# Kernel optimization log

Measured on AMD Instinct MI355X. Metric: run time of the kernel, lower is better.

## Reference

```python
import jax, jax.numpy as jnp
import numpy as np

B, N1, N2, D, H = 16, 1024, 1024, 1024, 16
DH = D // H  # head dim = 64
NEG = jnp.float32(-1e30)  # mask fill value (avoids -inf NaNs, bf16-safe)


def setup_inputs() -> dict:
    key = jax.random.key(0)
    ks = jax.random.split(key, 8)
    s = 0.02
    q = jax.random.normal(ks[0], (B, N1, D), dtype=jnp.float32)
    x = jax.random.normal(ks[1], (B, N2, D), dtype=jnp.float32)
    Wq = jax.random.normal(ks[2], (D, D), dtype=jnp.float32) * s
    Wk = jax.random.normal(ks[3], (D, D), dtype=jnp.float32) * s
    Wv = jax.random.normal(ks[4], (D, D), dtype=jnp.float32) * s
    Wo = jax.random.normal(ks[5], (D, D), dtype=jnp.float32) * s
    bq = jnp.zeros((D,), jnp.float32)
    bk = jnp.zeros((D,), jnp.float32)
    bv = jnp.zeros((D,), jnp.float32)
    bo = jnp.zeros((D,), jnp.float32)
    adj_mat = jax.random.randint(ks[6], (N1, N2), 0, 2).astype(jnp.bool_)
    return {"q": q, "x": x, "Wq": Wq, "bq": bq, "Wk": Wk, "bk": bk,
            "Wv": Wv, "bv": bv, "Wo": Wo, "bo": bo, "adj_mat": adj_mat}


def reference(q, x, Wq, bq, Wk, bk, Wv, bv, Wo, bo, adj_mat):
    b = q.shape[0]
    # QKV projections (torch Linear: y = x @ W.T + b), split into heads
    qh = (q @ Wq.T + bq).reshape(b, N1, H, DH).transpose(0, 2, 1, 3)  # [B,H,N1,DH]
    kh = (x @ Wk.T + bk).reshape(b, N2, H, DH).transpose(0, 2, 1, 3)  # [B,H,N2,DH]
    vh = (x @ Wv.T + bv).reshape(b, N2, H, DH).transpose(0, 2, 1, 3)  # [B,H,N2,DH]
    # masked SDPA with fixed adjacency mask (broadcast over batch & heads)
    scale = jnp.asarray(DH, qh.dtype) ** -0.5
    scores = jnp.einsum("bhqd,bhkd->bhqk", qh, kh) * scale           # [B,H,N1,N2]
    scores = jnp.where(adj_mat, scores, NEG)
    attn = jax.nn.softmax(scores, axis=-1)
    o = jnp.einsum("bhqk,bhkd->bhqd", attn, vh)                      # [B,H,N1,DH]
    o = o.transpose(0, 2, 1, 3).reshape(b, N1, D)
    return o @ Wo.T + bo
```

## Files before the change

### kernel.cpp

```cpp
#include <hip/hip_runtime.h>


typedef float f32x4 __attribute__((ext_vector_type(4)));
typedef __bf16 bf16x8 __attribute__((ext_vector_type(8)));

#define QSCALE 0.18033688f

__device__ __forceinline__ unsigned short f2bf(float f) {
    unsigned u = __builtin_bit_cast(unsigned, f);
    unsigned r = u + 0x7fffu + ((u >> 16) & 1u);
    return (unsigned short)(r >> 16);
}
__device__ __forceinline__ unsigned pk2(float a, float b) {
    return (unsigned)f2bf(a) | ((unsigned)f2bf(b) << 16);
}

__global__ __launch_bounds__(256) void cvt_bf16(const float* __restrict__ src,
                                                unsigned short* __restrict__ dst,
                                                int n8) {
    const int idx = blockIdx.x * 256 + threadIdx.x;
    if (idx >= n8) return;
    float4 a = ((const float4*)src)[idx * 2];
    float4 b = ((const float4*)src)[idx * 2 + 1];
    uint4 u;
    u.x = pk2(a.x, a.y); u.y = pk2(a.z, a.w);
    u.z = pk2(b.x, b.y); u.w = pk2(b.z, b.w);
    ((uint4*)dst)[idx] = u;
}

__global__ __launch_bounds__(256) void cvt_w4(const float* __restrict__ W0,
                                              const float* __restrict__ W1,
                                              const float* __restrict__ W2,
                                              const float* __restrict__ W3,
                                              unsigned short* __restrict__ o0,
                                              unsigned short* __restrict__ o1,
                                              unsigned short* __restrict__ o2,
                                              unsigned short* __restrict__ o3) {
    const float* s = (blockIdx.y == 0) ? W0 : (blockIdx.y == 1) ? W1
                   : (blockIdx.y == 2) ? W2 : W3;
    unsigned short* d = (blockIdx.y == 0) ? o0 : (blockIdx.y == 1) ? o1
                      : (blockIdx.y == 2) ? o2 : o3;
    const int idx = blockIdx.x * 256 + threadIdx.x;
    float4 a = ((const float4*)s)[idx * 2];
    float4 b = ((const float4*)s)[idx * 2 + 1];
    uint4 u;
    u.x = pk2(a.x, a.y); u.y = pk2(a.z, a.w);
    u.z = pk2(b.x, b.y); u.w = pk2(b.z, b.w);
    ((uint4*)d)[idx] = u;
}

template <int OUTM>
__global__ __launch_bounds__(256) void gemm_lds(const unsigned short* __restrict__ A,
                                                const unsigned short* __restrict__ W,
                                                const float* __restrict__ bias,
                                                void* __restrict__ Cp,
                                                float scale) {
    constexpr int N = 1024, K = 1024;
    __shared__ unsigned short As[128 * 64];
    __shared__ unsigned short Bs[128 * 64];

    const int t    = threadIdx.x;
    const int wave = t >> 6;
    const int lane = t & 63;
    const int bid  = blockIdx.x;
    const int xcd  = bid & 7;
    const int jj   = bid >> 3;
    const int n0   = (jj & 7) * 128;
    const int m0   = (xcd * 16 + (jj >> 3)) * 128;
    const int wr   = (wave >> 1) * 64;
    const int wc   = (wave & 1) * 64;
    const int lm   = lane & 15;
    const int quad = lane >> 4;

    int aoff[4], boff[4];
#pragma unroll
    for (int i = 0; i < 4; i++) {
        const int slot = wave * 256 + i * 64 + lane;
        const int r = slot >> 3;
        const int csrc = (slot & 7) ^ (r & 7);
        aoff[i] = (m0 + r) * K + csrc * 8;
        boff[i] = (n0 + r) * K + csrc * 8;
    }

    f32x4 acc[4][4] = {};

    for (int k0 = 0; k0 < K; k0 += 64) {
#pragma unroll
        for (int i = 0; i < 4; i++) {
            __builtin_amdgcn_global_load_lds(
                (const __attribute__((address_space(1))) unsigned int*)(A + aoff[i] + k0),
                (__attribute__((address_space(3))) unsigned int*)((char*)As + wave * 4096 + i * 1024),
                16, 0, 0);
            __builtin_amdgcn_global_load_lds(
                (const __attribute__((address_space(1))) unsigned int*)(W + boff[i] + k0),
                (__attribute__((address_space(3))) unsigned int*)((char*)Bs + wave * 4096 + i * 1024),
                16, 0, 0);
        }
        __syncthreads();

        bf16x8 af[2][4], bfr[2][4];
#pragma unroll
        for (int ks = 0; ks < 2; ks++)
#pragma unroll
            for (int i = 0; i < 4; i++) {
                const int pos = ((ks * 4 + quad) ^ (lm & 7)) * 16;
                af[ks][i]  = *(const bf16x8*)((const char*)As + (wr + i * 16 + lm) * 128 + pos);
                bfr[ks][i] = *(const bf16x8*)((const char*)Bs + (wc + i * 16 + lm) * 128 + pos);
            }
#pragma unroll
        for (int ks = 0; ks < 2; ks++)
#pragma unroll
            for (int i = 0; i < 4; i++)
#pragma unroll
                for (int j = 0; j < 4; j++)
                    acc[i][j] = __builtin_amdgcn_mfma_f32_16x16x32_bf16(af[ks][i], bfr[ks][j],
                                                                        acc[i][j], 0, 0, 0);
        __syncthreads();
    }

#pragma unroll
    for (int i = 0; i < 4; i++) {
        const int row = m0 + wr + i * 16 + quad * 4;
#pragma unroll
        for (int j = 0; j < 4; j++) {
            const int col = n0 + wc + j * 16 + lm;
            const float bb = bias[col];
            if constexpr (OUTM == 2) {
                const int bi = row >> 10, n2 = row & 1023;
                const int hh = col >> 6, dh = col & 63;
                uint2 pkd;
                pkd.x = pk2((acc[i][j][0] + bb) * scale, (acc[i][j][1] + bb) * scale);
                pkd.y = pk2((acc[i][j][2] + bb) * scale, (acc[i][j][3] + bb) * scale);
                *(uint2*)&((unsigned short*)Cp)[((size_t)((bi * 16 + hh) * 64 + dh) << 10) + n2] = pkd;
            } else {
#pragma unroll
                for (int rr = 0; rr < 4; rr++) {
                    const float v = (acc[i][j][rr] + bb) * scale;
                    if constexpr (OUTM == 0)
                        ((unsigned short*)Cp)[(size_t)(row + rr) * N + col] = f2bf(v);
                    else
                        ((float*)Cp)[(size_t)(row + rr) * N + col] = v;
                }
            }
        }
    }
}

template <bool A_BF16, int OUTM>
__global__ __launch_bounds__(256) void gemm_bt(const void* __restrict__ Ap,
                                               const float* __restrict__ Wp,
                                               const float* __restrict__ bias,
                                               void* __restrict__ Cp,
                                               float scale) {
    constexpr int N = 1024, K = 1024;
    __shared__ unsigned short As[128 * 40];
    __shared__ unsigned short Bs[128 * 40];

    const int t    = threadIdx.x;
    const int n0   = blockIdx.x * 128;
    const int m0   = blockIdx.y * 128;
    const int wave = t >> 6;
    const int lane = t & 63;
    const int wr   = (wave >> 1) * 64;
    const int wc   = (wave & 1) * 64;
    const int lm   = lane & 15;
    const int quad = lane >> 4;
    const int kfr  = quad * 8;
    const int srow  = t >> 1;
    const int shalf = (t & 1) * 16;

    f32x4 acc[4][4] = {};

    for (int k0 = 0; k0 < K; k0 += 32) {
        {
            unsigned short* dst = &As[srow * 40 + shalf];
            if constexpr (A_BF16) {
                const unsigned short* pa =
                    (const unsigned short*)Ap + (size_t)(m0 + srow) * K + k0 + shalf;
                *(uint4*)dst       = *(const uint4*)pa;
                *(uint4*)(dst + 8) = *(const uint4*)(pa + 8);
            } else {
                const float* pa = (const float*)Ap + (size_t)(m0 + srow) * K + k0 + shalf;
                float4 f0 = *(const float4*)(pa + 0);
                float4 f1 = *(const float4*)(pa + 4);
                float4 f2 = *(const float4*)(pa + 8);
                float4 f3 = *(const float4*)(pa + 12);
                uint4 u0, u1;
                u0.x = pk2(f0.x, f0.y); u0.y = pk2(f0.z, f0.w);
                u0.z = pk2(f1.x, f1.y); u0.w = pk2(f1.z, f1.w);
                u1.x = pk2(f2.x, f2.y); u1.y = pk2(f2.z, f2.w);
                u1.z = pk2(f3.x, f3.y); u1.w = pk2(f3.z, f3.w);
                *(uint4*)dst       = u0;
                *(uint4*)(dst + 8) = u1;
            }
        }
        {
            const float* pb = Wp + (size_t)(n0 + srow) * K + k0 + shalf;
            float4 f0 = *(const float4*)(pb + 0);
            float4 f1 = *(const float4*)(pb + 4);
            float4 f2 = *(const float4*)(pb + 8);
            float4 f3 = *(const float4*)(pb + 12);
            uint4 u0, u1;
            u0.x = pk2(f0.x, f0.y); u0.y = pk2(f0.z, f0.w);
            u0.z = pk2(f1.x, f1.y); u0.w = pk2(f1.z, f1.w);
            u1.x = pk2(f2.x, f2.y); u1.y = pk2(f2.z, f2.w);
            u1.z = pk2(f3.x, f3.y); u1.w = pk2(f3.z, f3.w);
            unsigned short* dst = &Bs[srow * 40 + shalf];
            *(uint4*)dst       = u0;
            *(uint4*)(dst + 8) = u1;
        }
        __syncthreads();

        bf16x8 af[4], bfr[4];
#pragma unroll
        for (int i = 0; i < 4; i++)
            af[i] = *reinterpret_cast<const bf16x8*>(&As[(wr + i * 16 + lm) * 40 + kfr]);
#pragma unroll
        for (int j = 0; j < 4; j++)
            bfr[j] = *reinterpret_cast<const bf16x8*>(&Bs[(wc + j * 16 + lm) * 40 + kfr]);
#pragma unroll
        for (int i = 0; i < 4; i++)
#pragma unroll
            for (int j = 0; j < 4; j++)
                acc[i][j] = __builtin_amdgcn_mfma_f32_16x16x32_bf16(af[i], bfr[j],
                                                                    acc[i][j], 0, 0, 0);
        __syncthreads();
    }

#pragma unroll
    for (int i = 0; i < 4; i++) {
        const int row = m0 + wr + i * 16 + quad * 4;
#pragma unroll
        for (int j = 0; j < 4; j++) {
            const int col = n0 + wc + j * 16 + lm;
            const float bb = bias[col];
#pragma unroll
            for (int rr = 0; rr < 4; rr++) {
                const float v = (acc[i][j][rr] + bb) * scale;
                const int m = row + rr;
                if constexpr (OUTM == 0) {
                    ((unsigned short*)Cp)[(size_t)m * N + col] = f2bf(v);
                } else if constexpr (OUTM == 1) {
                    ((float*)Cp)[(size_t)m * N + col] = v;
                } else {
                    const int bi = m >> 10, n2 = m & 1023;
                    const int hh = col >> 6, dh = col & 63;
                    ((unsigned short*)Cp)[((size_t)((bi * 16 + hh) * 64 + dh) << 10) + n2] =
                        f2bf(v);
                }
            }
        }
    }
}

__global__ __launch_bounds__(256) void pack_adj(const int* __restrict__ adj,
                                                unsigned* __restrict__ adjm) {
    const int idx = blockIdx.x * 256 + threadIdx.x;
    const int* src = adj + (size_t)idx * 32;
    unsigned w = 0;
#pragma unroll
    for (int i = 0; i < 32; i++) w |= (src[i] != 0 ? 1u : 0u) << i;
    adjm[idx] = w;
}

__global__ __launch_bounds__(256, 3) void attn_kernel(const unsigned short* __restrict__ Q,
                                                      const unsigned short* __restrict__ K,
                                                      const unsigned short* __restrict__ Vt,
                                                      const unsigned* __restrict__ adjm,
                                                      unsigned short* __restrict__ O) {
    __shared__ unsigned short Kbuf[2][4096];
    __shared__ unsigned short Vbuf[2][4096];
    __shared__ unsigned short Ps[4][2][16][72];

    const int t    = threadIdx.x;
    const int wave = t >> 6;
    const int lane = t & 63;
    const int lml  = lane & 15;
    const int quad = lane >> 4;

    const int bid   = blockIdx.x;
    const int xcd   = bid & 7;
    const int jj    = bid >> 3;
    const int group = xcd * 32 + (jj >> 3);
    const int q0    = (jj & 7) * 128;
    const int h     = group & 15;
    const int b     = group >> 4;

    int    ldofs[2];
    size_t kofs[2], vofs[2];
#pragma unroll
    for (int i = 0; i < 2; i++) {
        const int slot = i * 256 + t;
        const int r    = slot >> 3;
        const int cs   = (slot & 7) ^ (r & 7);
        ldofs[i] = slot * 16;
        kofs[i]  = (size_t)(b * 1024 + r) * 1024 + h * 64 + cs * 8;
        vofs[i]  = ((size_t)((b * 16 + h) * 64 + r) << 10) + cs * 8;
    }

    bf16x8 aq[2][2];
#pragma unroll
    for (int g = 0; g < 2; g++) {
        const unsigned short* qp =
            Q + ((size_t)(b * 1024 + q0 + wave * 32 + g * 16 + lml) * 1024 + h * 64 + quad * 8);
        aq[g][0] = __builtin_bit_cast(bf16x8, *(const uint4*)qp);
        aq[g][1] = __builtin_bit_cast(bf16x8, *(const uint4*)(qp + 32));
    }

    bf16x8 bones;
    {
        const unsigned short o1 = (lml == 0) ? (unsigned short)0x3F80 : (unsigned short)0;
        const unsigned oo = (unsigned)o1 | ((unsigned)o1 << 16);
        uint4 u; u.x = oo; u.y = oo; u.z = oo; u.w = oo;
        bones = __builtin_bit_cast(bf16x8, u);
    }

    f32x4 of[2][4] = {};
    f32x4 ol[2] = {};

    auto STAGE = [&](int bi, int c) {
        const size_t j0 = (size_t)c * 64;
#pragma unroll
        for (int i = 0; i < 2; i++) {
            __builtin_amdgcn_global_load_lds(
                (const __attribute__((address_space(1))) unsigned int*)(K + kofs[i] + j0 * 1024),
                (__attribute__((address_space(3))) unsigned int*)((char*)&Kbuf[bi][0] + ldofs[i]),
                16, 0, 0);
            __builtin_amdgcn_global_load_lds(
                (const __attribute__((address_space(1))) unsigned int*)(Vt + vofs[i] + j0),
                (__attribute__((address_space(3))) unsigned int*)((char*)&Vbuf[bi][0] + ldofs[i]),
                16, 0, 0);
        }
    };

    STAGE(0, 0);
    __syncthreads();

    int bi = 0;
    for (int c = 0; c < 16; ++c) {
        uint2 mw[2][4];
#pragma unroll
        for (int g = 0; g < 2; g++)
#pragma unroll
            for (int rr = 0; rr < 4; rr++) {
                const int row = q0 + wave * 32 + g * 16 + quad * 4 + rr;
                mw[g][rr] = *(const uint2*)&adjm[(size_t)row * 32 + c * 2];
            }

        if (c < 15) STAGE(bi ^ 1, c + 1);

        bf16x8 bk[4][2];
#pragma unroll
        for (int f = 0; f < 4; f++)
#pragma unroll
            for (int ks = 0; ks < 2; ks++) {
                const int row = f * 16 + lml;
                const int pos = ((ks * 4 + quad) ^ (lml & 7)) * 16;
                bk[f][ks] = *(const bf16x8*)((const char*)&Kbuf[bi][0] + row * 128 + pos);
            }

        f32x4 sf[2][4] = {};
        __builtin_amdgcn_s_setprio(1);
#pragma unroll
        for (int g = 0; g < 2; g++)
#pragma unroll
            for (int f = 0; f < 4; f++)
#pragma unroll
                for (int ks = 0; ks < 2; ks++)
                    sf[g][f] = __builtin_amdgcn_mfma_f32_16x16x32_bf16(aq[g][ks], bk[f][ks],
                                                                       sf[g][f], 0, 0, 0);
        __builtin_amdgcn_s_setprio(0);

#pragma unroll
        for (int g = 0; g < 2; g++)
#pragma unroll
            for (int rr = 0; rr < 4; rr++) {
                const unsigned w0s = mw[g][rr].x >> lml;
                const unsigned w1s = mw[g][rr].y >> lml;
#pragma unroll
                for (int f = 0; f < 4; f++) {
                    const unsigned ws  = (f < 2) ? w0s : w1s;
                    const unsigned bit = (f & 1) ? ((ws >> 16) & 1u) : (ws & 1u);
                    const float p = bit ? __builtin_amdgcn_exp2f(sf[g][f][rr]) : 0.0f;
                    Ps[wave][g][quad * 4 + rr][f * 16 + lml] =
                        (unsigned short)(__builtin_bit_cast(unsigned, p) >> 16);
                }
            }

        bf16x8 bv[4][2];
#pragma unroll
        for (int f = 0; f < 4; f++)
#pragma unroll
            for (int ks = 0; ks < 2; ks++) {
                const int row = f * 16 + lml;
                const int pos = ((ks * 4 + quad) ^ (lml & 7)) * 16;
                bv[f][ks] = *(const bf16x8*)((const char*)&Vbuf[bi][0] + row * 128 + pos);
            }

#pragma unroll
        for (int g = 0; g < 2; g++) {
            const bf16x8 ap0 = *reinterpret_cast<const bf16x8*>(&Ps[wave][g][lml][quad * 8]);
            const bf16x8 ap1 = *reinterpret_cast<const bf16x8*>(&Ps[wave][g][lml][32 + quad * 8]);
            __builtin_amdgcn_s_setprio(1);
#pragma unroll
            for (int f = 0; f < 4; f++) {
                of[g][f] = __builtin_amdgcn_mfma_f32_16x16x32_bf16(ap0, bv[f][0], of[g][f], 0, 0, 0);
                of[g][f] = __builtin_amdgcn_mfma_f32_16x16x32_bf16(ap1, bv[f][1], of[g][f], 0, 0, 0);
            }
            ol[g] = __builtin_amdgcn_mfma_f32_16x16x32_bf16(ap0, bones, ol[g], 0, 0, 0);
            ol[g] = __builtin_amdgcn_mfma_f32_16x16x32_bf16(ap1, bones, ol[g], 0, 0, 0);
            __builtin_amdgcn_s_setprio(0);
        }

        __syncthreads();
        bi ^= 1;
    }

#pragma unroll
    for (int g = 0; g < 2; g++) {
        float inv[4];
#pragma unroll
        for (int rr = 0; rr < 4; rr++)
            inv[rr] = 1.0f / __shfl(ol[g][rr], lane & 48);
#pragma unroll
        for (int f = 0; f < 4; f++)
#pragma unroll
            for (int rr = 0; rr < 4; rr++) {
                const size_t row = (size_t)(b * 1024 + q0 + wave * 32 + g * 16 + quad * 4 + rr);
                O[row * 1024 + h * 64 + f * 16 + lml] = f2bf(of[g][f][rr] * inv[rr]);
            }
    }
}

extern "C" void kernel_launch(void* const* d_in, const int* in_sizes, int n_in,
                              void* d_out, int out_size, void* d_ws, size_t ws_size,
                              hipStream_t stream) {
    const float* q  = (const float*)d_in[0];
    const float* x  = (const float*)d_in[1];
    const float* Wq = (const float*)d_in[2];
    const float* bq = (const float*)d_in[3];
    const float* Wk = (const float*)d_in[4];
    const float* bk = (const float*)d_in[5];
    const float* Wv = (const float*)d_in[6];
    const float* bv = (const float*)d_in[7];
    const float* Wo = (const float*)d_in[8];
    const float* bo = (const float*)d_in[9];
    const int* adj  = (const int*)d_in[10];
    float* out = (float*)d_out;

    const size_t MB = 1024 * 1024;
    const size_t NELEM = (size_t)16 * MB;
    char* w = (char*)d_ws;

    dim3 gswz(1024), tb(256);
    const size_t FULL_WS = 168 * MB + 128 * 1024;

    if (ws_size >= FULL_WS) {
        unsigned short* qb  = (unsigned short*)(w);
        unsigned short* xb  = (unsigned short*)(w + 32 * MB);
        unsigned short* Wqb = (unsigned short*)(w + 64 * MB);
        unsigned short* Wkb = (unsigned short*)(w + 66 * MB);
        unsigned short* Wvb = (unsigned short*)(w + 68 * MB);
        unsigned short* Wob = (unsigned short*)(w + 70 * MB);
        unsigned short* Qb  = (unsigned short*)(w + 72 * MB);
        unsigned short* Kb  = (unsigned short*)(w + 104 * MB);
        unsigned short* Vtb = (unsigned short*)(w + 136 * MB);
        unsigned* adjm      = (unsigned*)(w + 168 * MB);
        unsigned short* Ob  = qb;

        hipLaunchKernelGGL(cvt_bf16, dim3(8192), tb, 0, stream, q, qb, (int)(NELEM / 8));
        hipLaunchKernelGGL(cvt_bf16, dim3(8192), tb, 0, stream, x, xb, (int)(NELEM / 8));
        hipLaunchKernelGGL(cvt_w4, dim3(512, 4), tb, 0, stream, Wq, Wk, Wv, Wo,
                           Wqb, Wkb, Wvb, Wob);
        hipLaunchKernelGGL(pack_adj, dim3(128), tb, 0, stream, adj, adjm);

        hipLaunchKernelGGL((gemm_lds<0>), gswz, tb, 0, stream, qb, Wqb, bq, (void*)Qb, QSCALE);
        hipLaunchKernelGGL((gemm_lds<0>), gswz, tb, 0, stream, xb, Wkb, bk, (void*)Kb, 1.0f);
        hipLaunchKernelGGL((gemm_lds<2>), gswz, tb, 0, stream, xb, Wvb, bv, (void*)Vtb, 1.0f);
        hipLaunchKernelGGL(attn_kernel, dim3(2048), tb, 0, stream, Qb, Kb, Vtb, adjm, Ob);
        hipLaunchKernelGGL((gemm_lds<1>), gswz, tb, 0, stream, Ob, Wob, bo, (void*)out, 1.0f);
    } else {
        unsigned short* Qb  = (unsigned short*)(w);
        unsigned short* Kb  = (unsigned short*)(w + 32 * MB);
        unsigned short* Vtb = (unsigned short*)(w + 64 * MB);
        unsigned short* Ob  = (unsigned short*)(w + 96 * MB);
        unsigned* adjm      = (unsigned*)(w + 128 * MB);

        hipLaunchKernelGGL(pack_adj, dim3(128), tb, 0, stream, adj, adjm);
        hipLaunchKernelGGL((gemm_bt<false, 0>), dim3(8, 128), tb, 0, stream,
                           (const void*)q, Wq, bq, (void*)Qb, QSCALE);
        hipLaunchKernelGGL((gemm_bt<false, 0>), dim3(8, 128), tb, 0, stream,
                           (const void*)x, Wk, bk, (void*)Kb, 1.0f);
        hipLaunchKernelGGL((gemm_bt<false, 2>), dim3(8, 128), tb, 0, stream,
                           (const void*)x, Wv, bv, (void*)Vtb, 1.0f);
        hipLaunchKernelGGL(attn_kernel, dim3(2048), tb, 0, stream, Qb, Kb, Vtb, adjm, Ob);
        hipLaunchKernelGGL((gemm_bt<true, 1>), dim3(8, 128), tb, 0, stream,
                           (const void*)Ob, Wo, bo, (void*)out, 1.0f);
    }
}
```

Baseline: 480.9 us.

## Use 32x32 MFMA with transposed scores and register permlane P transpose

Switches the attention kernel from 16x16x32 to 32x32x16 bf16 MFMA. It computes the scores transposed (K as the A operand) so each lane's P values can be packed with v_cvt_pk_bf16_f32 and rearranged with v_permlane32_swap into the A operand of the PV MFMA. This removes the per-wave shared-memory Ps round trip and its LDS writes and reads. The row-sum MFMA now uses an all-ones operand, and the mask is applied by clamping to -1e30 before exp2, replacing the branch. The trade-off is higher register pressure from 16-wide accumulators and reliance on the exact lane mappings of the inline asm for correctness.

```diff
diff --git a/kernel.cpp b/kernel.cpp
--- a/kernel.cpp
+++ b/kernel.cpp
@@ -2,6 +2,7 @@
 
 
 typedef float f32x4 __attribute__((ext_vector_type(4)));
+typedef float f32x16 __attribute__((ext_vector_type(16)));
 typedef __bf16 bf16x8 __attribute__((ext_vector_type(8)));
 
 #define QSCALE 0.18033688f
@@ -270,13 +271,12 @@
                                                       unsigned short* __restrict__ O) {
     __shared__ unsigned short Kbuf[2][4096];
     __shared__ unsigned short Vbuf[2][4096];
-    __shared__ unsigned short Ps[4][2][16][72];
 
     const int t    = threadIdx.x;
     const int wave = t >> 6;
     const int lane = t & 63;
-    const int lml  = lane & 15;
-    const int quad = lane >> 4;
+    const int l32  = lane & 31;
+    const int hi   = lane >> 5;
 
     const int bid   = blockIdx.x;
     const int xcd   = bid & 7;
@@ -286,6 +286,8 @@
     const int h     = group & 15;
     const int b     = group >> 4;
 
+    const int qrow = q0 + wave * 32 + l32;
+
     int    ldofs[2];
     size_t kofs[2], vofs[2];
 #pragma unroll
@@ -298,25 +300,22 @@
         vofs[i]  = ((size_t)((b * 16 + h) * 64 + r) << 10) + cs * 8;
     }
 
-    bf16x8 aq[2][2];
-#pragma unroll
-    for (int g = 0; g < 2; g++) {
+    bf16x8 aq[4];
+    {
         const unsigned short* qp =
-            Q + ((size_t)(b * 1024 + q0 + wave * 32 + g * 16 + lml) * 1024 + h * 64 + quad * 8);
-        aq[g][0] = __builtin_bit_cast(bf16x8, *(const uint4*)qp);
-        aq[g][1] = __builtin_bit_cast(bf16x8, *(const uint4*)(qp + 32));
+            Q + ((size_t)(b * 1024 + qrow) * 1024 + h * 64 + hi * 8);
+#pragma unroll
+        for (int s = 0; s < 4; s++)
+            aq[s] = __builtin_bit_cast(bf16x8, *(const uint4*)(qp + s * 16));
     }
 
     bf16x8 bones;
     {
-        const unsigned short o1 = (lml == 0) ? (unsigned short)0x3F80 : (unsigned short)0;
-        const unsigned oo = (unsigned)o1 | ((unsigned)o1 << 16);
-        uint4 u; u.x = oo; u.y = oo; u.z = oo; u.w = oo;
+        uint4 u; u.x = 0x3F803F80u; u.y = u.x; u.z = u.x; u.w = u.x;
         bones = __builtin_bit_cast(bf16x8, u);
     }
 
-    f32x4 of[2][4] = {};
-    f32x4 ol[2] = {};
+    f32x16 of0 = {}, of1 = {}, ol = {};
 
     auto STAGE = [&](int bi, int c) {
         const size_t j0 = (size_t)c * 64;
@@ -338,97 +337,80 @@
 
     int bi = 0;
     for (int c = 0; c < 16; ++c) {
-        uint2 mw[2][4];
-#pragma unroll
-        for (int g = 0; g < 2; g++)
-#pragma unroll
-            for (int rr = 0; rr < 4; rr++) {
-                const int row = q0 + wave * 32 + g * 16 + quad * 4 + rr;
-                mw[g][rr] = *(const uint2*)&adjm[(size_t)row * 32 + c * 2];
-            }
+        const uint2 mw = *(const uint2*)&adjm[(size_t)qrow * 32 + c * 2];
 
         if (c < 15) STAGE(bi ^ 1, c + 1);
 
-        bf16x8 bk[4][2];
-#pragma unroll
-        for (int f = 0; f < 4; f++)
-#pragma unroll
-            for (int ks = 0; ks < 2; ks++) {
-                const int row = f * 16 + lml;
-                const int pos = ((ks * 4 + quad) ^ (lml & 7)) * 16;
-                bk[f][ks] = *(const bf16x8*)((const char*)&Kbuf[bi][0] + row * 128 + pos);
-            }
-
-        f32x4 sf[2][4] = {};
+        f32x16 sf[2] = {{}, {}};
         __builtin_amdgcn_s_setprio(1);
 #pragma unroll
-        for (int g = 0; g < 2; g++)
-#pragma unroll
-            for (int f = 0; f < 4; f++)
-#pragma unroll
-                for (int ks = 0; ks < 2; ks++)
-                    sf[g][f] = __builtin_amdgcn_mfma_f32_16x16x32_bf16(aq[g][ks], bk[f][ks],
-                                                                       sf[g][f], 0, 0, 0);
+        for (int f = 0; f < 2; f++)
+#pragma unroll
+            for (int s = 0; s < 4; s++) {
+                const int pos = ((2 * s + hi) ^ (l32 & 7)) * 16;
+                const bf16x8 kf =
+                    *(const bf16x8*)((const char*)&Kbuf[bi][0] + (f * 32 + l32) * 128 + pos);
+                sf[f] = __builtin_amdgcn_mfma_f32_32x32x16_bf16(kf, aq[s], sf[f], 0, 0, 0);
+            }
         __builtin_amdgcn_s_setprio(0);
 
-#pragma unroll
-        for (int g = 0; g < 2; g++)
-#pragma unroll
-            for (int rr = 0; rr < 4; rr++) {
-                const unsigned w0s = mw[g][rr].x >> lml;
-                const unsigned w1s = mw[g][rr].y >> lml;
-#pragma unroll
-                for (int f = 0; f < 4; f++) {
-                    const unsigned ws  = (f < 2) ? w0s : w1s;
-                    const unsigned bit = (f & 1) ? ((ws >> 16) & 1u) : (ws & 1u);
-                    const float p = bit ? __builtin_amdgcn_exp2f(sf[g][f][rr]) : 0.0f;
-                    Ps[wave][g][quad * 4 + rr][f * 16 + lml] =
-                        (unsigned short)(__builtin_bit_cast(unsigned, p) >> 16);
+        unsigned d[2][4][2];
+#pragma unroll
+        for (int f = 0; f < 2; f++) {
+            const unsigned wh = ((f == 0) ? mw.x : mw.y) >> (hi * 4);
+            float p[16];
+#pragma unroll
+            for (int r = 0; r < 16; r++) {
+                const unsigned bit = (wh >> ((r & 3) + 8 * (r >> 2))) & 1u;
+                p[r] = __builtin_amdgcn_exp2f(bit ? sf[f][r] : -1e30f);
+            }
+#pragma unroll
+            for (int a = 0; a < 4; a++)
+#pragma unroll
+                for (int bb = 0; bb < 2; bb++) {
+                    unsigned dd;
+                    asm("v_cvt_pk_bf16_f32 %0, %1, %2"
+                        : "=v"(dd) : "v"(p[4 * a + 2 * bb]), "v"(p[4 * a + 2 * bb + 1]));
+                    d[f][a][bb] = dd;
                 }
-            }
-
-        bf16x8 bv[4][2];
-#pragma unroll
-        for (int f = 0; f < 4; f++)
-#pragma unroll
-            for (int ks = 0; ks < 2; ks++) {
-                const int row = f * 16 + lml;
-                const int pos = ((ks * 4 + quad) ^ (lml & 7)) * 16;
-                bv[f][ks] = *(const bf16x8*)((const char*)&Vbuf[bi][0] + row * 128 + pos);
-            }
-
-#pragma unroll
-        for (int g = 0; g < 2; g++) {
-            const bf16x8 ap0 = *reinterpret_cast<const bf16x8*>(&Ps[wave][g][lml][quad * 8]);
-            const bf16x8 ap1 = *reinterpret_cast<const bf16x8*>(&Ps[wave][g][lml][32 + quad * 8]);
-            __builtin_amdgcn_s_setprio(1);
-#pragma unroll
-            for (int f = 0; f < 4; f++) {
-                of[g][f] = __builtin_amdgcn_mfma_f32_16x16x32_bf16(ap0, bv[f][0], of[g][f], 0, 0, 0);
-                of[g][f] = __builtin_amdgcn_mfma_f32_16x16x32_bf16(ap1, bv[f][1], of[g][f], 0, 0, 0);
-            }
-            ol[g] = __builtin_amdgcn_mfma_f32_16x16x32_bf16(ap0, bones, ol[g], 0, 0, 0);
-            ol[g] = __builtin_amdgcn_mfma_f32_16x16x32_bf16(ap1, bones, ol[g], 0, 0, 0);
-            __builtin_amdgcn_s_setprio(0);
-        }
+        }
+
+        bf16x8 tA[4];
+#pragma unroll
+        for (int s = 0; s < 4; s++) {
+            const int f = s >> 1, sg = s & 1;
+            unsigned A0 = d[f][2 * sg][0], B0 = d[f][2 * sg + 1][0];
+            unsigned A1 = d[f][2 * sg][1], B1 = d[f][2 * sg + 1][1];
+            asm("v_permlane32_swap_b32 %0, %1" : "+v"(A0), "+v"(B0));
+            asm("v_permlane32_swap_b32 %0, %1" : "+v"(A1), "+v"(B1));
+            uint4 td; td.x = A0; td.y = A1; td.z = B0; td.w = B1;
+            tA[s] = __builtin_bit_cast(bf16x8, td);
+        }
+
+        __builtin_amdgcn_s_setprio(1);
+#pragma unroll
+        for (int s = 0; s < 4; s++) {
+            const int pos = ((2 * s + hi) ^ (l32 & 7)) * 16;
+            const bf16x8 v0 = *(const bf16x8*)((const char*)&Vbuf[bi][0] + l32 * 128 + pos);
+            const bf16x8 v1 = *(const bf16x8*)((const char*)&Vbuf[bi][0] + (32 + l32) * 128 + pos);
+            of0 = __builtin_amdgcn_mfma_f32_32x32x16_bf16(tA[s], v0, of0, 0, 0, 0);
+            of1 = __builtin_amdgcn_mfma_f32_32x32x16_bf16(tA[s], v1, of1, 0, 0, 0);
+            ol  = __builtin_amdgcn_mfma_f32_32x32x16_bf16(tA[s], bones, ol, 0, 0, 0);
+        }
+        __builtin_amdgcn_s_setprio(0);
 
         __syncthreads();
         bi ^= 1;
     }
 
 #pragma unroll
-    for (int g = 0; g < 2; g++) {
-        float inv[4];
-#pragma unroll
-        for (int rr = 0; rr < 4; rr++)
-            inv[rr] = 1.0f / __shfl(ol[g][rr], lane & 48);
-#pragma unroll
-        for (int f = 0; f < 4; f++)
-#pragma unroll
-            for (int rr = 0; rr < 4; rr++) {
-                const size_t row = (size_t)(b * 1024 + q0 + wave * 32 + g * 16 + quad * 4 + rr);
-                O[row * 1024 + h * 64 + f * 16 + lml] = f2bf(of[g][f][rr] * inv[rr]);
-            }
+    for (int r = 0; r < 16; r++) {
+        const float iv = 1.0f / ol[r];
+        const size_t row = (size_t)(b * 1024 + q0 + wave * 32 +
+                                    (r & 3) + 8 * (r >> 2) + 4 * hi);
+        unsigned short* op = O + row * 1024 + h * 64 + l32;
+        op[0]  = f2bf(of0[r] * iv);
+        op[32] = f2bf(of1[r] * iv);
     }
 }
 
```

After: 474.9 us. Within noise of the previous version (-1.2%).
